# Kernel optimization log

Hardware: AMD Instinct MI355X
Metric: run time of the kernel (lower is better)

The kernel has to match this reference:

```python
import jax, jax.numpy as jnp
import numpy as np
import math

H = 8          # n_head
MAX_POS = 48   # block_size / max_positions
MAX_PART = 16  # max_particles


def _rel_bias(table, L, max_len):
    # table: (2*max_len-1, H). Equivalent to the tile/view trick in
    # SimpleRelativePositionalBias: bias[h, i, j] = b[j - i + L - 1, h]
    b = table[max_len - L: max_len + L - 1]          # (2L-1, H)
    idx = jnp.arange(L)
    rel = idx[None, :] - idx[:, None] + (L - 1)      # (L, L) in [0, 2L-2]
    return jnp.transpose(b[rel], (2, 0, 1))          # (H, L, L)


def setup_inputs() -> dict:
    key = jax.random.key(0)
    ks = jax.random.split(key, 7)
    B, N, T, C = 16, 16, 48, 512
    s = 0.02
    return {
        "x": jax.random.normal(ks[0], (B, N, T, C), jnp.float32),
        "Wq": jax.random.normal(ks[1], (C, C), jnp.float32) * s,
        "Wk": jax.random.normal(ks[2], (C, C), jnp.float32) * s,
        "Wv": jax.random.normal(ks[3], (C, C), jnp.float32) * s,
        "Wo": jax.random.normal(ks[4], (C, C), jnp.float32) * s,
        "rel_pos_bias": jax.random.normal(ks[5], (2 * MAX_POS - 1, H), jnp.float32) * s,
        "particle_rel_pos_bias": jax.random.normal(ks[6], (2 * MAX_PART - 1, H), jnp.float32) * s,
    }


def reference(x, Wq, Wk, Wv, Wo, rel_pos_bias, particle_rel_pos_bias):
    B, N, T, C = x.shape
    hd = C // H
    L = N * T
    xf = x.reshape(B, L, C)
    # (B, H, L, hd) each; Linear with no bias
    q = (xf @ Wq).reshape(B, L, H, hd).transpose(0, 2, 1, 3)
    k = (xf @ Wk).reshape(B, L, H, hd).transpose(0, 2, 1, 3)
    v = (xf @ Wv).reshape(B, L, H, hd).transpose(0, 2, 1, 3)

    att = jnp.einsum('bhqd,bhkd->bhqk', q, k) * (1.0 / math.sqrt(hd))
    att = att.reshape(B, H, N, T, N, T)

    bias_t = _rel_bias(rel_pos_bias, T, MAX_POS).reshape(1, H, 1, T, 1, T)
    bias_p = _rel_bias(particle_rel_pos_bias, N, MAX_PART).reshape(1, H, N, 1, N, 1)
    att = att + bias_t + bias_p

    # causal over the time axes only (all particles at allowed times visible)
    causal = jnp.tril(jnp.ones((T, T), dtype=bool))
    att = jnp.where(causal[None, None, None, :, None, :], att, -jnp.inf)

    att = jax.nn.softmax(att.reshape(B, H, L, L), axis=-1)
    y = att @ v                                      # (B, H, L, hd)
    y = y.transpose(0, 2, 1, 3).reshape(B, L, C) @ Wo
    return y.reshape(B, N, T, C)
```

## Files before the change

### kernel.cpp

```cpp
#include <hip/hip_runtime.h>
#include <hip/hip_bf16.h>
#include <math.h>

#define B_  16
#define N_  16
#define T_  48
#define C_  512
#define H_  8
#define HD_ 64
#define L_  768
#define BL_ 12288

typedef __attribute__((ext_vector_type(8))) short b16x8;
typedef __attribute__((ext_vector_type(4))) float f32x4;
typedef __attribute__((ext_vector_type(2))) unsigned int u32x2;

__device__ __forceinline__ short f2b(float f) {
  __hip_bfloat16 h = __float2bfloat16(f);
  return *reinterpret_cast<short*>(&h);
}
__device__ __forceinline__ unsigned cvt_pk_bf16(float a, float b) {
  unsigned d;
  asm("v_cvt_pk_bf16_f32 %0, %1, %2" : "=v"(d) : "v"(a), "v"(b));
  return d;
}
__device__ __forceinline__ float ex2(float x) {
  float d;
  asm("v_exp_f32 %0, %1" : "=v"(d) : "v"(x));
  return d;
}
__device__ __forceinline__ void gload16(const void* g, void* l) {
  __builtin_amdgcn_global_load_lds(
      (const __attribute__((address_space(1))) void*)g,
      (__attribute__((address_space(3))) void*)l, 16, 0, 0);
}

__global__ __launch_bounds__(256) void prep_kernel(
    const float* __restrict__ x,
    const float* __restrict__ Wq, const float* __restrict__ Wk,
    const float* __restrict__ Wv, const float* __restrict__ Wo,
    short* __restrict__ xb, short* __restrict__ WT)
{
  __shared__ float tile[32][33];
  int blk = blockIdx.x;
  int tid = threadIdx.x;
  if (blk < 3072) {
    int i = blk * 256 + tid;
    const float4* src = (const float4*)(x + (size_t)i * 8);
    float4 a = src[0], b = src[1];
    short tmp[8] = {f2b(a.x), f2b(a.y), f2b(a.z), f2b(a.w),
                    f2b(b.x), f2b(b.y), f2b(b.z), f2b(b.w)};
    *(b16x8*)(xb + (size_t)i * 8) = *(b16x8*)tmp;
  } else {
    int idx = blk - 3072;
    int mat = idx >> 8, rem = idx & 255;
    const float* W = (mat == 0) ? Wq : (mat == 1) ? Wk : (mat == 2) ? Wv : Wo;
    float scale = (mat == 0) ? 0.18033688f : 1.0f;
    int k0 = (rem >> 4) * 32, n0 = (rem & 15) * 32;
    int tx = tid & 31, ty = tid >> 5;
    for (int i = ty; i < 32; i += 8) tile[i][tx] = W[(size_t)(k0 + i) * 512 + n0 + tx];
    __syncthreads();
    short* dst = WT + (size_t)mat * 262144;
    for (int i = ty; i < 32; i += 8)
      dst[(size_t)(n0 + i) * 512 + k0 + tx] = f2b(tile[tx][i] * scale);
  }
}

__global__ __launch_bounds__(256) void qkv_kernel(
    const short* __restrict__ xb, const short* __restrict__ WT,
    short* __restrict__ q2, short* __restrict__ k2, short* __restrict__ vT2)
{
  __shared__ __align__(16) short smem[16384];
  int tid = threadIdx.x;
  int w = tid >> 6, lane = tid & 63, n16 = lane & 15, quad = lane >> 4;
  int bm = blockIdx.x, bn = blockIdx.y;
  int mat = bn >> 2;
  int ncol0 = (bn & 3) * 128;
  const short* Wt = WT + (size_t)mat * 262144;
  int bq = bm / 6;
  int rr0 = (bm % 6) * 128;

  f32x4 zero4 = {0.f, 0.f, 0.f, 0.f};
  f32x4 acc[4][4];
  #pragma unroll
  for (int mt = 0; mt < 4; ++mt)
    #pragma unroll
    for (int nt = 0; nt < 4; ++nt) acc[mt][nt] = zero4;

  const short* gA[2];
  const short* gB[2];
  #pragma unroll
  for (int i = 0; i < 2; ++i) {
    int r16 = w + 4 * i;
    int rr = rr0 + r16 * 16 + (lane >> 2);
    int pt = rr >> 4, pn = rr & 15;
    gA[i] = xb + ((size_t)bq * 768 + pn * 48 + pt) * 512 + (lane & 3) * 8;
    gB[i] = Wt + (size_t)(ncol0 + r16 * 16 + (lane >> 2)) * 512 + (lane & 3) * 8;
  }
  int ldsoff = (w) * 512 + lane * 8;

  auto stage = [&](int buf, int kt) {
    short* As = smem + buf * 8192;
    short* Bs = As + 4096;
    #pragma unroll
    for (int i = 0; i < 2; ++i) {
      gload16(gA[i] + kt * 32, As + i * 2048 + ldsoff);
      gload16(gB[i] + kt * 32, Bs + i * 2048 + ldsoff);
    }
  };

  int wm = (w >> 1) * 64, wn = (w & 1) * 64;
  stage(0, 0);
  __syncthreads();
  int buf = 0;
  for (int kt = 0; kt < 16; ++kt) {
    if (kt < 15) stage(buf ^ 1, kt + 1);
    const short (*As)[32] = (const short(*)[32])(smem + buf * 8192);
    const short (*Bs)[32] = (const short(*)[32])(smem + buf * 8192 + 4096);
    b16x8 af[4], bf[4];
    #pragma unroll
    for (int mt = 0; mt < 4; ++mt) af[mt] = *(const b16x8*)&As[wm + mt * 16 + n16][quad * 8];
    #pragma unroll
    for (int nt = 0; nt < 4; ++nt) bf[nt] = *(const b16x8*)&Bs[wn + nt * 16 + n16][quad * 8];
    #pragma unroll
    for (int mt = 0; mt < 4; ++mt)
      #pragma unroll
      for (int nt = 0; nt < 4; ++nt)
        acc[mt][nt] = __builtin_amdgcn_mfma_f32_16x16x32_bf16(af[mt], bf[nt], acc[mt][nt], 0, 0, 0);
    __syncthreads();
    buf ^= 1;
  }

  short (*Ls)[136] = (short(*)[136])smem;
  for (int c = 0; c < 4; ++c) {
    __syncthreads();
    if ((w >> 1) == (c >> 1)) {
      int mtb = (c & 1) * 2;
      #pragma unroll
      for (int mi = 0; mi < 2; ++mi) {
        #pragma unroll
        for (int nt = 0; nt < 4; ++nt)
          #pragma unroll
          for (int r = 0; r < 4; ++r)
            Ls[mi * 16 + quad * 4 + r][wn + nt * 16 + n16] = f2b(acc[mtb + mi][nt][r]);
      }
    }
    __syncthreads();
    int rrc = rr0 + c * 32;
    if (mat != 2) {
      short* dst = (mat == 0) ? q2 : k2;
      int row = tid >> 3, c0 = (tid & 7) * 16;
      int hhg = (ncol0 + c0) >> 6, d0 = (ncol0 + c0) & 63;
      short* dp = dst + ((size_t)(bq * 8 + hhg) * 768 + rrc + row) * 64 + d0;
      *(b16x8*)dp       = *(b16x8*)&Ls[row][c0];
      *(b16x8*)(dp + 8) = *(b16x8*)&Ls[row][c0 + 8];
    } else {
      int cp = tid & 63, r8 = (tid >> 6) * 8;
      int c0 = 2 * cp;
      int hhg = (ncol0 + c0) >> 6, d0 = (ncol0 + c0) & 63;
      short t0[8], t1[8];
      #pragma unroll
      for (int j = 0; j < 8; ++j) { t0[j] = Ls[r8 + j][c0]; t1[j] = Ls[r8 + j][c0 + 1]; }
      short* dp = vT2 + ((size_t)(bq * 8 + hhg) * 64 + d0) * 768 + rrc + r8;
      *(b16x8*)dp         = *(b16x8*)t0;
      *(b16x8*)(dp + 768) = *(b16x8*)t1;
    }
  }
}

__global__ __launch_bounds__(256, 4) void attn_kernel(
    const short* __restrict__ q2, const short* __restrict__ k2,
    const short* __restrict__ vT2,
    const float* __restrict__ relT, const float* __restrict__ relP,
    short* __restrict__ yatt)
{
  __shared__ __align__(16) short KV[2][4096];
  __shared__ float btL[96];

  const float LOG2E = 1.44269504f;
  int tid = threadIdx.x;
  int w = tid >> 6, lane = tid & 63, n16 = lane & 15, quad = lane >> 4;
  int blk = blockIdx.x;
  int h = blk & 7;
  int g = blk >> 3;
  int pgg = g % 6, b = g / 6;
  int pairq = pgg * 4 + w;
  int qtA = pairq, qtB = 47 - pairq;
  int nAw = (qtA + 2) >> 1;
  int nBw = (qtB + 2) >> 1;
  int nBmax = 24 - 2 * pgg;

  if (tid < 96) btL[tid] = relT[(tid < 95 ? tid : 94) * 8 + h] * LOG2E;

  float bpT[4];
  #pragma unroll
  for (int r = 0; r < 4; ++r)
    bpT[r] = relP[(quad * 4 + r - n16 + 15) * 8 + h] * LOG2E;

  size_t bh = (size_t)(b * 8 + h);
  const short* qb = q2 + bh * 49152;
  const short* kb = k2 + bh * 49152;
  const short* vb = vT2 + bh * 49152;

  b16x8 qA0 = *(const b16x8*)(qb + (qtA * 16 + n16) * 64 + quad * 8);
  b16x8 qA1 = *(const b16x8*)(qb + (qtA * 16 + n16) * 64 + quad * 8 + 32);
  b16x8 qB0 = *(const b16x8*)(qb + (qtB * 16 + n16) * 64 + quad * 8);
  b16x8 qB1 = *(const b16x8*)(qb + (qtB * 16 + n16) * 64 + quad * 8 + 32);

  f32x4 zero4 = {0.f, 0.f, 0.f, 0.f};
  f32x4 oA[4], oB[4];
  float psA = 0.f, psB = 0.f;
  #pragma unroll
  for (int nt = 0; nt < 4; ++nt) { oA[nt] = zero4; oB[nt] = zero4; }

  int krow = tid >> 3, kc8 = tid & 7;
  int vd   = tid >> 2, vkc = tid & 3;
  int kdst = (kc8 < 4 ? 0 : 1024) + krow * 32 + (kc8 & 3) * 8;
  int vdst = 2048 + vd * 32 + vkc * 8;
  b16x8 s0, s2;
  auto LOADR = [&](int kt2) {
    s0 = *(const b16x8*)(kb + (size_t)(kt2 * 32 + krow) * 64 + kc8 * 8);
    s2 = *(const b16x8*)(vb + (size_t)vd * 768 + kt2 * 32 + vkc * 8);
  };
  auto WRITE = [&](int buf) {
    *(b16x8*)(KV[buf] + kdst) = s0;
    *(b16x8*)(KV[buf] + vdst) = s2;
  };

  auto exp_pack = [&](const f32x4& s0v, const f32x4& s1v, float bt0, float bt1,
                      float& ps) -> b16x8 {
    float e00 = ex2(s0v[0] + bt0 + bpT[0]);
    float e01 = ex2(s0v[1] + bt0 + bpT[1]);
    float e02 = ex2(s0v[2] + bt0 + bpT[2]);
    float e03 = ex2(s0v[3] + bt0 + bpT[3]);
    float e10 = ex2(s1v[0] + bt1 + bpT[0]);
    float e11 = ex2(s1v[1] + bt1 + bpT[1]);
    float e12 = ex2(s1v[2] + bt1 + bpT[2]);
    float e13 = ex2(s1v[3] + bt1 + bpT[3]);
    ps += ((e00 + e01) + (e02 + e03)) + ((e10 + e11) + (e12 + e13));
    unsigned p0 = cvt_pk_bf16(e00, e01);
    unsigned p1 = cvt_pk_bf16(e02, e03);
    unsigned p2 = cvt_pk_bf16(e10, e11);
    unsigned p3 = cvt_pk_bf16(e12, e13);
    u32x2 a02 = __builtin_amdgcn_permlane32_swap(p0, p2, false, false);
    u32x2 z02 = __builtin_amdgcn_permlane16_swap(a02.x, a02.y, false, false);
    u32x2 a13 = __builtin_amdgcn_permlane32_swap(p1, p3, false, false);
    u32x2 z13 = __builtin_amdgcn_permlane16_swap(a13.x, a13.y, false, false);
    union { unsigned u[4]; b16x8 v; } r;
    r.u[0] = z02.x;
    r.u[1] = z13.x;
    r.u[2] = z02.y;
    r.u[3] = z13.y;
    return r.v;
  };

  LOADR(0);
  WRITE(0);
  __syncthreads();

  int buf = 0;
  for (int kt2 = 0; kt2 < nBmax; ++kt2) {
    bool more = (kt2 + 1 < nBmax);
    if (more) LOADR(kt2 + 1);

    bool doB = kt2 < nBw;
    bool doA = kt2 < nAw;
    if (doB) {
      const short* p = KV[buf];
      b16x8 kf0 = *(const b16x8*)(p + n16 * 32 + quad * 8);
      b16x8 kf1 = *(const b16x8*)(p + 1024 + n16 * 32 + quad * 8);
      b16x8 kf2 = *(const b16x8*)(p + (16 + n16) * 32 + quad * 8);
      b16x8 kf3 = *(const b16x8*)(p + 1024 + (16 + n16) * 32 + quad * 8);
      b16x8 vf0 = *(const b16x8*)(p + 2048 + n16 * 32 + quad * 8);
      b16x8 vf1 = *(const b16x8*)(p + 2048 + (16 + n16) * 32 + quad * 8);
      b16x8 vf2 = *(const b16x8*)(p + 2048 + (32 + n16) * 32 + quad * 8);
      b16x8 vf3 = *(const b16x8*)(p + 2048 + (48 + n16) * 32 + quad * 8);

      int kt0 = kt2 * 2;
      __builtin_amdgcn_s_setprio(1);
      f32x4 sB0 = zero4, sB1 = zero4;
      sB0 = __builtin_amdgcn_mfma_f32_16x16x32_bf16(kf0, qB0, sB0, 0, 0, 0);
      sB0 = __builtin_amdgcn_mfma_f32_16x16x32_bf16(kf1, qB1, sB0, 0, 0, 0);
      sB1 = __builtin_amdgcn_mfma_f32_16x16x32_bf16(kf2, qB0, sB1, 0, 0, 0);
      sB1 = __builtin_amdgcn_mfma_f32_16x16x32_bf16(kf3, qB1, sB1, 0, 0, 0);
      f32x4 sA0 = zero4, sA1 = zero4;
      if (doA) {
        sA0 = __builtin_amdgcn_mfma_f32_16x16x32_bf16(kf0, qA0, sA0, 0, 0, 0);
        sA0 = __builtin_amdgcn_mfma_f32_16x16x32_bf16(kf1, qA1, sA0, 0, 0, 0);
        sA1 = __builtin_amdgcn_mfma_f32_16x16x32_bf16(kf2, qA0, sA1, 0, 0, 0);
        sA1 = __builtin_amdgcn_mfma_f32_16x16x32_bf16(kf3, qA1, sA1, 0, 0, 0);
      }
      __builtin_amdgcn_s_setprio(0);
      float btB0 = (kt0 <= qtB) ? btL[kt0 - qtB + 47] : -1e30f;
      float btB1 = (kt0 + 1 <= qtB) ? btL[kt0 + 1 - qtB + 47] : -1e30f;
      b16x8 pfB = exp_pack(sB0, sB1, btB0, btB1, psB);
      __builtin_amdgcn_s_setprio(1);
      oB[0] = __builtin_amdgcn_mfma_f32_16x16x32_bf16(pfB, vf0, oB[0], 0, 0, 0);
      oB[1] = __builtin_amdgcn_mfma_f32_16x16x32_bf16(pfB, vf1, oB[1], 0, 0, 0);
      oB[2] = __builtin_amdgcn_mfma_f32_16x16x32_bf16(pfB, vf2, oB[2], 0, 0, 0);
      oB[3] = __builtin_amdgcn_mfma_f32_16x16x32_bf16(pfB, vf3, oB[3], 0, 0, 0);
      __builtin_amdgcn_s_setprio(0);
      if (doA) {
        float btA0 = (kt0 <= qtA) ? btL[kt0 - qtA + 47] : -1e30f;
        float btA1 = (kt0 + 1 <= qtA) ? btL[kt0 + 1 - qtA + 47] : -1e30f;
        b16x8 pfA = exp_pack(sA0, sA1, btA0, btA1, psA);
        __builtin_amdgcn_s_setprio(1);
        oA[0] = __builtin_amdgcn_mfma_f32_16x16x32_bf16(pfA, vf0, oA[0], 0, 0, 0);
        oA[1] = __builtin_amdgcn_mfma_f32_16x16x32_bf16(pfA, vf1, oA[1], 0, 0, 0);
        oA[2] = __builtin_amdgcn_mfma_f32_16x16x32_bf16(pfA, vf2, oA[2], 0, 0, 0);
        oA[3] = __builtin_amdgcn_mfma_f32_16x16x32_bf16(pfA, vf3, oA[3], 0, 0, 0);
        __builtin_amdgcn_s_setprio(0);
      }
    }

    if (more) WRITE(buf ^ 1);
    __syncthreads();
    buf ^= 1;
  }

  psA += __shfl_xor(psA, 16); psA += __shfl_xor(psA, 32);
  psB += __shfl_xor(psB, 16); psB += __shfl_xor(psB, 32);
  float invA = 1.0f / psA, invB = 1.0f / psB;
  float pnA[4], pnB[4];
  #pragma unroll
  for (int r = 0; r < 4; ++r) {
    pnA[r] = __shfl(invA, quad * 4 + r);
    pnB[r] = __shfl(invB, quad * 4 + r);
  }

  #pragma unroll
  for (int nt = 0; nt < 4; ++nt) {
    int c = h * 64 + nt * 16 + n16;
    #pragma unroll
    for (int r = 0; r < 4; ++r) {
      int qn = quad * 4 + r;
      yatt[((size_t)b * 768 + qn * 48 + qtA) * 512 + c] = f2b(oA[nt][r] * pnA[r]);
      yatt[((size_t)b * 768 + qn * 48 + qtB) * 512 + c] = f2b(oB[nt][r] * pnB[r]);
    }
  }
}

__global__ __launch_bounds__(256) void proj_kernel(
    const short* __restrict__ yatt, const short* __restrict__ WT,
    float* __restrict__ out)
{
  __shared__ __align__(16) short smem[16384];
  int tid = threadIdx.x;
  int w = tid >> 6, lane = tid & 63, n16 = lane & 15, quad = lane >> 4;
  int row0 = blockIdx.x * 128;
  int ncol0 = blockIdx.y * 128;
  const short* Wt = WT + (size_t)3 * 262144;

  f32x4 zero4 = {0.f, 0.f, 0.f, 0.f};
  f32x4 acc[4][4];
  #pragma unroll
  for (int mt = 0; mt < 4; ++mt)
    #pragma unroll
    for (int nt = 0; nt < 4; ++nt) acc[mt][nt] = zero4;

  const short* gA[2];
  const short* gB[2];
  #pragma unroll
  for (int i = 0; i < 2; ++i) {
    int r16 = w + 4 * i;
    gA[i] = yatt + (size_t)(row0 + r16 * 16 + (lane >> 2)) * 512 + (lane & 3) * 8;
    gB[i] = Wt + (size_t)(ncol0 + r16 * 16 + (lane >> 2)) * 512 + (lane & 3) * 8;
  }
  int ldsoff = w * 512 + lane * 8;

  auto stage = [&](int buf, int kt) {
    short* As = smem + buf * 8192;
    short* Bs = As + 4096;
    #pragma unroll
    for (int i = 0; i < 2; ++i) {
      gload16(gA[i] + kt * 32, As + i * 2048 + ldsoff);
      gload16(gB[i] + kt * 32, Bs + i * 2048 + ldsoff);
    }
  };

  int wm = (w >> 1) * 64, wn = (w & 1) * 64;
  stage(0, 0);
  __syncthreads();
  int buf = 0;
  for (int kt = 0; kt < 16; ++kt) {
    if (kt < 15) stage(buf ^ 1, kt + 1);
    const short (*As)[32] = (const short(*)[32])(smem + buf * 8192);
    const short (*Bs)[32] = (const short(*)[32])(smem + buf * 8192 + 4096);
    b16x8 af[4], bf[4];
    #pragma unroll
    for (int mt = 0; mt < 4; ++mt) af[mt] = *(const b16x8*)&As[wm + mt * 16 + n16][quad * 8];
    #pragma unroll
    for (int nt = 0; nt < 4; ++nt) bf[nt] = *(const b16x8*)&Bs[wn + nt * 16 + n16][quad * 8];
    #pragma unroll
    for (int mt = 0; mt < 4; ++mt)
      #pragma unroll
      for (int nt = 0; nt < 4; ++nt)
        acc[mt][nt] = __builtin_amdgcn_mfma_f32_16x16x32_bf16(af[mt], bf[nt], acc[mt][nt], 0, 0, 0);
    __syncthreads();
    buf ^= 1;
  }

  #pragma unroll
  for (int mt = 0; mt < 4; ++mt) {
    int rowb = row0 + wm + mt * 16 + quad * 4;
    #pragma unroll
    for (int nt = 0; nt < 4; ++nt) {
      int colg = ncol0 + wn + nt * 16 + n16;
      #pragma unroll
      for (int r = 0; r < 4; ++r)
        out[(size_t)(rowb + r) * 512 + colg] = acc[mt][nt][r];
    }
  }
}

extern "C" void kernel_launch(void* const* d_in, const int* in_sizes, int n_in,
                              void* d_out, int out_size, void* d_ws, size_t ws_size,
                              hipStream_t stream) {
  const float* x    = (const float*)d_in[0];
  const float* Wq   = (const float*)d_in[1];
  const float* Wk   = (const float*)d_in[2];
  const float* Wv   = (const float*)d_in[3];
  const float* Wo   = (const float*)d_in[4];
  const float* relT = (const float*)d_in[5];
  const float* relP = (const float*)d_in[6];

  char* wsb = (char*)d_ws;
  const size_t SZ = (size_t)BL_ * C_ * 2;
  short* xb  = (short*)(wsb);
  short* WT  = (short*)(wsb + SZ);
  short* qb  = (short*)(wsb + SZ + 2097152);
  short* kb  = (short*)(wsb + 2 * SZ + 2097152);
  short* vTb = (short*)(wsb + 3 * SZ + 2097152);
  short* yat = (short*)(wsb + 4 * SZ + 2097152 + 4096);

  prep_kernel<<<dim3(4096), dim3(256), 0, stream>>>(x, Wq, Wk, Wv, Wo, xb, WT);
  qkv_kernel<<<dim3(96, 12), dim3(256), 0, stream>>>(xb, WT, qb, kb, vTb);
  attn_kernel<<<dim3(768), dim3(256), 0, stream>>>(qb, kb, vTb, relT, relP, yat);
  proj_kernel<<<dim3(96, 4), dim3(256), 0, stream>>>(yat, WT, (float*)d_out);
}
```

Baseline: 156.9 us.

## Process two KV tiles per sync in attention and halve proj tile width

```diff
diff --git a/kernel.cpp b/kernel.cpp
--- a/kernel.cpp
+++ b/kernel.cpp
@@ -168,13 +168,13 @@
   }
 }
 
-__global__ __launch_bounds__(256, 4) void attn_kernel(
+__global__ __launch_bounds__(256, 3) void attn_kernel(
     const short* __restrict__ q2, const short* __restrict__ k2,
     const short* __restrict__ vT2,
     const float* __restrict__ relT, const float* __restrict__ relP,
     short* __restrict__ yatt)
 {
-  __shared__ __align__(16) short KV[2][4096];
+  __shared__ __align__(16) short KV[2][2][4096];
   __shared__ float btL[96];
 
   const float LOG2E = 1.44269504f;
@@ -189,6 +189,7 @@
   int nAw = (qtA + 2) >> 1;
   int nBw = (qtB + 2) >> 1;
   int nBmax = 24 - 2 * pgg;
+  int nRounds = nBmax >> 1;
 
   if (tid < 96) btL[tid] = relT[(tid < 95 ? tid : 94) * 8 + h] * LOG2E;
 
@@ -217,14 +218,14 @@
   int vd   = tid >> 2, vkc = tid & 3;
   int kdst = (kc8 < 4 ? 0 : 1024) + krow * 32 + (kc8 & 3) * 8;
   int vdst = 2048 + vd * 32 + vkc * 8;
-  b16x8 s0, s2;
-  auto LOADR = [&](int kt2) {
-    s0 = *(const b16x8*)(kb + (size_t)(kt2 * 32 + krow) * 64 + kc8 * 8);
-    s2 = *(const b16x8*)(vb + (size_t)vd * 768 + kt2 * 32 + vkc * 8);
-  };
-  auto WRITE = [&](int buf) {
-    *(b16x8*)(KV[buf] + kdst) = s0;
-    *(b16x8*)(KV[buf] + vdst) = s2;
+  b16x8 sk0, sv0, sk1, sv1;
+  auto LOADR = [&](int kt2, b16x8& sk, b16x8& sv) {
+    sk = *(const b16x8*)(kb + (size_t)(kt2 * 32 + krow) * 64 + kc8 * 8);
+    sv = *(const b16x8*)(vb + (size_t)vd * 768 + kt2 * 32 + vkc * 8);
+  };
+  auto WRITE = [&](short* p, const b16x8& sk, const b16x8& sv) {
+    *(b16x8*)(p + kdst) = sk;
+    *(b16x8*)(p + vdst) = sv;
   };
 
   auto exp_pack = [&](const f32x4& s0v, const f32x4& s1v, float bt0, float bt1,
@@ -254,66 +255,69 @@
     return r.v;
   };
 
-  LOADR(0);
-  WRITE(0);
+  auto step = [&](int kt2, const short* p) {
+    bool doB = kt2 < nBw;
+    if (!doB) return;
+    bool doA = kt2 < nAw;
+    b16x8 kf0 = *(const b16x8*)(p + n16 * 32 + quad * 8);
+    b16x8 kf1 = *(const b16x8*)(p + 1024 + n16 * 32 + quad * 8);
+    b16x8 kf2 = *(const b16x8*)(p + (16 + n16) * 32 + quad * 8);
+    b16x8 kf3 = *(const b16x8*)(p + 1024 + (16 + n16) * 32 + quad * 8);
+    b16x8 vf0 = *(const b16x8*)(p + 2048 + n16 * 32 + quad * 8);
+    b16x8 vf1 = *(const b16x8*)(p + 2048 + (16 + n16) * 32 + quad * 8);
+    b16x8 vf2 = *(const b16x8*)(p + 2048 + (32 + n16) * 32 + quad * 8);
+    b16x8 vf3 = *(const b16x8*)(p + 2048 + (48 + n16) * 32 + quad * 8);
+
+    int kt0 = kt2 * 2;
+    f32x4 sB0 = zero4, sB1 = zero4;
+    sB0 = __builtin_amdgcn_mfma_f32_16x16x32_bf16(kf0, qB0, sB0, 0, 0, 0);
+    sB0 = __builtin_amdgcn_mfma_f32_16x16x32_bf16(kf1, qB1, sB0, 0, 0, 0);
+    sB1 = __builtin_amdgcn_mfma_f32_16x16x32_bf16(kf2, qB0, sB1, 0, 0, 0);
+    sB1 = __builtin_amdgcn_mfma_f32_16x16x32_bf16(kf3, qB1, sB1, 0, 0, 0);
+    f32x4 sA0 = zero4, sA1 = zero4;
+    if (doA) {
+      sA0 = __builtin_amdgcn_mfma_f32_16x16x32_bf16(kf0, qA0, sA0, 0, 0, 0);
+      sA0 = __builtin_amdgcn_mfma_f32_16x16x32_bf16(kf1, qA1, sA0, 0, 0, 0);
+      sA1 = __builtin_amdgcn_mfma_f32_16x16x32_bf16(kf2, qA0, sA1, 0, 0, 0);
+      sA1 = __builtin_amdgcn_mfma_f32_16x16x32_bf16(kf3, qA1, sA1, 0, 0, 0);
+    }
+    float btB0 = (kt0 <= qtB) ? btL[kt0 - qtB + 47] : -1e30f;
+    float btB1 = (kt0 + 1 <= qtB) ? btL[kt0 + 1 - qtB + 47] : -1e30f;
+    b16x8 pfB = exp_pack(sB0, sB1, btB0, btB1, psB);
+    oB[0] = __builtin_amdgcn_mfma_f32_16x16x32_bf16(pfB, vf0, oB[0], 0, 0, 0);
+    oB[1] = __builtin_amdgcn_mfma_f32_16x16x32_bf16(pfB, vf1, oB[1], 0, 0, 0);
+    oB[2] = __builtin_amdgcn_mfma_f32_16x16x32_bf16(pfB, vf2, oB[2], 0, 0, 0);
+    oB[3] = __builtin_amdgcn_mfma_f32_16x16x32_bf16(pfB, vf3, oB[3], 0, 0, 0);
+    if (doA) {
+      float btA0 = (kt0 <= qtA) ? btL[kt0 - qtA + 47] : -1e30f;
+      float btA1 = (kt0 + 1 <= qtA) ? btL[kt0 + 1 - qtA + 47] : -1e30f;
+      b16x8 pfA = exp_pack(sA0, sA1, btA0, btA1, psA);
+      oA[0] = __builtin_amdgcn_mfma_f32_16x16x32_bf16(pfA, vf0, oA[0], 0, 0, 0);
+      oA[1] = __builtin_amdgcn_mfma_f32_16x16x32_bf16(pfA, vf1, oA[1], 0, 0, 0);
+      oA[2] = __builtin_amdgcn_mfma_f32_16x16x32_bf16(pfA, vf2, oA[2], 0, 0, 0);
+      oA[3] = __builtin_amdgcn_mfma_f32_16x16x32_bf16(pfA, vf3, oA[3], 0, 0, 0);
+    }
+  };
+
+  LOADR(0, sk0, sv0);
+  LOADR(1, sk1, sv1);
+  WRITE(&KV[0][0][0], sk0, sv0);
+  WRITE(&KV[0][1][0], sk1, sv1);
   __syncthreads();
 
   int buf = 0;
-  for (int kt2 = 0; kt2 < nBmax; ++kt2) {
-    bool more = (kt2 + 1 < nBmax);
-    if (more) LOADR(kt2 + 1);
-
-    bool doB = kt2 < nBw;
-    bool doA = kt2 < nAw;
-    if (doB) {
-      const short* p = KV[buf];
-      b16x8 kf0 = *(const b16x8*)(p + n16 * 32 + quad * 8);
-      b16x8 kf1 = *(const b16x8*)(p + 1024 + n16 * 32 + quad * 8);
-      b16x8 kf2 = *(const b16x8*)(p + (16 + n16) * 32 + quad * 8);
-      b16x8 kf3 = *(const b16x8*)(p + 1024 + (16 + n16) * 32 + quad * 8);
-      b16x8 vf0 = *(const b16x8*)(p + 2048 + n16 * 32 + quad * 8);
-      b16x8 vf1 = *(const b16x8*)(p + 2048 + (16 + n16) * 32 + quad * 8);
-      b16x8 vf2 = *(const b16x8*)(p + 2048 + (32 + n16) * 32 + quad * 8);
-      b16x8 vf3 = *(const b16x8*)(p + 2048 + (48 + n16) * 32 + quad * 8);
-
-      int kt0 = kt2 * 2;
-      __builtin_amdgcn_s_setprio(1);
-      f32x4 sB0 = zero4, sB1 = zero4;
-      sB0 = __builtin_amdgcn_mfma_f32_16x16x32_bf16(kf0, qB0, sB0, 0, 0, 0);
-      sB0 = __builtin_amdgcn_mfma_f32_16x16x32_bf16(kf1, qB1, sB0, 0, 0, 0);
-      sB1 = __builtin_amdgcn_mfma_f32_16x16x32_bf16(kf2, qB0, sB1, 0, 0, 0);
-      sB1 = __builtin_amdgcn_mfma_f32_16x16x32_bf16(kf3, qB1, sB1, 0, 0, 0);
-      f32x4 sA0 = zero4, sA1 = zero4;
-      if (doA) {
-        sA0 = __builtin_amdgcn_mfma_f32_16x16x32_bf16(kf0, qA0, sA0, 0, 0, 0);
-        sA0 = __builtin_amdgcn_mfma_f32_16x16x32_bf16(kf1, qA1, sA0, 0, 0, 0);
-        sA1 = __builtin_amdgcn_mfma_f32_16x16x32_bf16(kf2, qA0, sA1, 0, 0, 0);
-        sA1 = __builtin_amdgcn_mfma_f32_16x16x32_bf16(kf3, qA1, sA1, 0, 0, 0);
-      }
-      __builtin_amdgcn_s_setprio(0);
-      float btB0 = (kt0 <= qtB) ? btL[kt0 - qtB + 47] : -1e30f;
-      float btB1 = (kt0 + 1 <= qtB) ? btL[kt0 + 1 - qtB + 47] : -1e30f;
-      b16x8 pfB = exp_pack(sB0, sB1, btB0, btB1, psB);
-      __builtin_amdgcn_s_setprio(1);
-      oB[0] = __builtin_amdgcn_mfma_f32_16x16x32_bf16(pfB, vf0, oB[0], 0, 0, 0);
-      oB[1] = __builtin_amdgcn_mfma_f32_16x16x32_bf16(pfB, vf1, oB[1], 0, 0, 0);
-      oB[2] = __builtin_amdgcn_mfma_f32_16x16x32_bf16(pfB, vf2, oB[2], 0, 0, 0);
-      oB[3] = __builtin_amdgcn_mfma_f32_16x16x32_bf16(pfB, vf3, oB[3], 0, 0, 0);
-      __builtin_amdgcn_s_setprio(0);
-      if (doA) {
-        float btA0 = (kt0 <= qtA) ? btL[kt0 - qtA + 47] : -1e30f;
-        float btA1 = (kt0 + 1 <= qtA) ? btL[kt0 + 1 - qtA + 47] : -1e30f;
-        b16x8 pfA = exp_pack(sA0, sA1, btA0, btA1, psA);
-        __builtin_amdgcn_s_setprio(1);
-        oA[0] = __builtin_amdgcn_mfma_f32_16x16x32_bf16(pfA, vf0, oA[0], 0, 0, 0);
-        oA[1] = __builtin_amdgcn_mfma_f32_16x16x32_bf16(pfA, vf1, oA[1], 0, 0, 0);
-        oA[2] = __builtin_amdgcn_mfma_f32_16x16x32_bf16(pfA, vf2, oA[2], 0, 0, 0);
-        oA[3] = __builtin_amdgcn_mfma_f32_16x16x32_bf16(pfA, vf3, oA[3], 0, 0, 0);
-        __builtin_amdgcn_s_setprio(0);
-      }
-    }
-
-    if (more) WRITE(buf ^ 1);
+  for (int r = 0; r < nRounds; ++r) {
+    bool more = (r + 1 < nRounds);
+    if (more) {
+      LOADR(2 * r + 2, sk0, sv0);
+      LOADR(2 * r + 3, sk1, sv1);
+    }
+    step(2 * r,     &KV[buf][0][0]);
+    step(2 * r + 1, &KV[buf][1][0]);
+    if (more) {
+      WRITE(&KV[buf ^ 1][0][0], sk0, sv0);
+      WRITE(&KV[buf ^ 1][1][0], sk1, sv1);
+    }
     __syncthreads();
     buf ^= 1;
   }
@@ -344,57 +348,55 @@
     const short* __restrict__ yatt, const short* __restrict__ WT,
     float* __restrict__ out)
 {
-  __shared__ __align__(16) short smem[16384];
+  __shared__ __align__(16) short smem[12288];
   int tid = threadIdx.x;
   int w = tid >> 6, lane = tid & 63, n16 = lane & 15, quad = lane >> 4;
   int row0 = blockIdx.x * 128;
-  int ncol0 = blockIdx.y * 128;
+  int ncol0 = blockIdx.y * 64;
   const short* Wt = WT + (size_t)3 * 262144;
 
   f32x4 zero4 = {0.f, 0.f, 0.f, 0.f};
-  f32x4 acc[4][4];
+  f32x4 acc[4][2];
   #pragma unroll
   for (int mt = 0; mt < 4; ++mt)
     #pragma unroll
-    for (int nt = 0; nt < 4; ++nt) acc[mt][nt] = zero4;
+    for (int nt = 0; nt < 2; ++nt) acc[mt][nt] = zero4;
 
   const short* gA[2];
-  const short* gB[2];
   #pragma unroll
   for (int i = 0; i < 2; ++i) {
     int r16 = w + 4 * i;
     gA[i] = yatt + (size_t)(row0 + r16 * 16 + (lane >> 2)) * 512 + (lane & 3) * 8;
-    gB[i] = Wt + (size_t)(ncol0 + r16 * 16 + (lane >> 2)) * 512 + (lane & 3) * 8;
-  }
+  }
+  const short* gB = Wt + (size_t)(ncol0 + w * 16 + (lane >> 2)) * 512 + (lane & 3) * 8;
   int ldsoff = w * 512 + lane * 8;
 
   auto stage = [&](int buf, int kt) {
-    short* As = smem + buf * 8192;
+    short* As = smem + buf * 6144;
     short* Bs = As + 4096;
     #pragma unroll
-    for (int i = 0; i < 2; ++i) {
+    for (int i = 0; i < 2; ++i)
       gload16(gA[i] + kt * 32, As + i * 2048 + ldsoff);
-      gload16(gB[i] + kt * 32, Bs + i * 2048 + ldsoff);
-    }
-  };
-
-  int wm = (w >> 1) * 64, wn = (w & 1) * 64;
+    gload16(gB + kt * 32, Bs + ldsoff);
+  };
+
+  int wm = (w >> 1) * 64, wn = (w & 1) * 32;
   stage(0, 0);
   __syncthreads();
   int buf = 0;
   for (int kt = 0; kt < 16; ++kt) {
     if (kt < 15) stage(buf ^ 1, kt + 1);
-    const short (*As)[32] = (const short(*)[32])(smem + buf * 8192);
-    const short (*Bs)[32] = (const short(*)[32])(smem + buf * 8192 + 4096);
-    b16x8 af[4], bf[4];
+    const short (*As)[32] = (const short(*)[32])(smem + buf * 6144);
+    const short (*Bs)[32] = (const short(*)[32])(smem + buf * 6144 + 4096);
+    b16x8 af[4], bf[2];
     #pragma unroll
     for (int mt = 0; mt < 4; ++mt) af[mt] = *(const b16x8*)&As[wm + mt * 16 + n16][quad * 8];
     #pragma unroll
-    for (int nt = 0; nt < 4; ++nt) bf[nt] = *(const b16x8*)&Bs[wn + nt * 16 + n16][quad * 8];
+    for (int nt = 0; nt < 2; ++nt) bf[nt] = *(const b16x8*)&Bs[wn + nt * 16 + n16][quad * 8];
     #pragma unroll
     for (int mt = 0; mt < 4; ++mt)
       #pragma unroll
-      for (int nt = 0; nt < 4; ++nt)
+      for (int nt = 0; nt < 2; ++nt)
         acc[mt][nt] = __builtin_amdgcn_mfma_f32_16x16x32_bf16(af[mt], bf[nt], acc[mt][nt], 0, 0, 0);
     __syncthreads();
     buf ^= 1;
@@ -404,7 +406,7 @@
   for (int mt = 0; mt < 4; ++mt) {
     int rowb = row0 + wm + mt * 16 + quad * 4;
     #pragma unroll
-    for (int nt = 0; nt < 4; ++nt) {
+    for (int nt = 0; nt < 2; ++nt) {
       int colg = ncol0 + wn + nt * 16 + n16;
       #pragma unroll
       for (int r = 0; r < 4; ++r)
@@ -436,5 +438,5 @@
   prep_kernel<<<dim3(4096), dim3(256), 0, stream>>>(x, Wq, Wk, Wv, Wo, xb, WT);
   qkv_kernel<<<dim3(96, 12), dim3(256), 0, stream>>>(xb, WT, qb, kb, vTb);
   attn_kernel<<<dim3(768), dim3(256), 0, stream>>>(qb, kb, vTb, relT, relP, yat);
-  proj_kernel<<<dim3(96, 4), dim3(256), 0, stream>>>(yat, WT, (float*)d_out);
-}
+  proj_kernel<<<dim3(96, 8), dim3(256), 0, stream>>>(yat, WT, (float*)d_out);
+}
```

Measured after the change: 158.3 us. No clear change (+0.9%).
